# Performance work log

Hardware: AMD Instinct MI355X
Metric: run time of the kernel (lower is better)

The kernel has to match this reference:

```python
import jax, jax.numpy as jnp
import numpy as np

N_BUCKETS = 512
SLOTS_PER_BUCKET = 32
TAU = 0.1
ALPHA = 0.5


def _l2norm(x, eps=1e-12):
    return x / jnp.maximum(jnp.linalg.norm(x, axis=-1, keepdims=True), eps)


def setup_inputs() -> dict:
    key = jax.random.key(0)
    ks = jax.random.split(key, 6)
    B, T, D = 2, 2048, 1024
    total_slots = N_BUCKETS * SLOTS_PER_BUCKET
    vocab = 50257
    query_emb = jax.random.normal(ks[0], (B, T, D), dtype=jnp.float32)
    tids = jax.random.randint(ks[1], (B, T), 0, vocab)
    slot_keys = jax.random.normal(ks[2], (total_slots, D), dtype=jnp.float32)
    slot_values = jax.random.normal(ks[3], (total_slots, D), dtype=jnp.float32)
    slot_tids = jax.random.randint(ks[4], (total_slots,), 0, vocab)
    centroid_codebook = _l2norm(jax.random.normal(ks[5], (N_BUCKETS, D), dtype=jnp.float32))
    return {
        "query_emb": query_emb,
        "tids": tids,
        "slot_keys": slot_keys,
        "slot_values": slot_values,
        "slot_tids": slot_tids,
        "centroid_codebook": centroid_codebook,
    }


def reference(query_emb, tids, slot_keys, slot_values, slot_tids, centroid_codebook):
    # CentroidAddressableManifold.read
    buckets = tids % N_BUCKETS                                  # [B,T]
    lex_anchors = centroid_codebook[buckets]                    # [B,T,D]
    q_norm = _l2norm(query_emb)
    # bucket-indexed gather of 32 slots per token
    indices = buckets[..., None] * SLOTS_PER_BUCKET + jnp.arange(SLOTS_PER_BUCKET)  # [B,T,S]
    b_keys = slot_keys[indices]                                 # [B,T,S,D]
    b_vals = slot_values[indices]                               # [B,T,S,D]
    unified_query = _l2norm(ALPHA * q_norm + (1.0 - ALPHA) * lex_anchors)
    scores = jnp.einsum("btd,btsd->bts", unified_query, b_keys)  # [B,T,S]
    # hard-match path
    gathered_tids = slot_tids[indices]                          # [B,T,S]
    match_mask = (tids[..., None] == gathered_tids).astype(scores.dtype)
    match_sum = match_mask.sum(axis=-1, keepdims=True)
    has_match = match_sum > 0
    probs_hard = match_mask / (match_sum + 1e-9)
    probs_soft = jax.nn.softmax(scores / TAU, axis=-1)
    val_hard = jnp.einsum("bts,btsw->btw", probs_hard, b_vals)
    val_soft = jnp.einsum("bts,btsw->btw", probs_soft, b_vals)
    val_out = jnp.where(has_match, val_hard, val_soft)          # [B,T,D]
    return val_out
```

## Files before the change

kernel.cpp:

```cpp
#include <hip/hip_runtime.h>

#define NB 512
#define SLOTS 32
#define D 1024
#define D4 256
#define TC 8
#define CAP 64
#define TAU_INV 10.0f
#define BT 512

__global__ void k_zero(int* __restrict__ cnt) {
    if (threadIdx.x < NB) cnt[threadIdx.x] = 0;
}

__global__ void k_build(const int* __restrict__ tids, int n,
                        int* __restrict__ cnt, int* __restrict__ list) {
    int i = blockIdx.x * 256 + threadIdx.x;
    if (i < n) {
        int b = tids[i] & (NB - 1);
        int p = atomicAdd(&cnt[b], 1);
        if (p < CAP) list[b * CAP + p] = i;
    }
}

__global__ __launch_bounds__(BT, 2)
void k_main(const float* __restrict__ query,
            const int*   __restrict__ tids,
            const float* __restrict__ skeys,
            const float* __restrict__ svals,
            const int*   __restrict__ stids,
            const float* __restrict__ centroid,
            float*       __restrict__ out,
            const int*   __restrict__ cnt,
            const int*   __restrict__ list)
{
    const int bucket = blockIdx.x & (NB - 1);
    const int part   = blockIdx.x >> 9;
    const int tidx   = threadIdx.x;
    const int lane   = tidx & 63;
    const int wid    = tidx >> 6;

    const int count = min(cnt[bucket], CAP);
    const int ncnt  = (count - part + 1) >> 1;
    if (ncnt <= 0) return;

    __shared__ float s_uq[TC][D];
    __shared__ float s_scores[TC][SLOTS];
    __shared__ float s_probs[TC][SLOTS];
    __shared__ int   s_tok[TC];
    __shared__ int   s_ttid[TC];

    const int slot_tid = stids[bucket * SLOTS + (lane & 31)];
    const float4* kb = (const float4*)(skeys + (size_t)bucket * SLOTS * D);
    const float4* vb = (const float4*)(svals + (size_t)bucket * SLOTS * D);
    const float4* cb = (const float4*)(centroid + (size_t)bucket * D);

    for (int c0 = 0; c0 < ncnt; c0 += TC) {
        const int nt = min(TC, ncnt - c0);

        if (wid < nt) {
            const int tok = list[bucket * CAP + part + 2 * (c0 + wid)];
            const float4* q4 = (const float4*)(query + (size_t)tok * D);
            float4 qv[4], anc[4];
            float ss = 0.f;
            #pragma unroll
            for (int j = 0; j < 4; ++j) {
                qv[j]  = q4[lane + 64 * j];
                anc[j] = cb[lane + 64 * j];
                ss += qv[j].x*qv[j].x + qv[j].y*qv[j].y + qv[j].z*qv[j].z + qv[j].w*qv[j].w;
            }
            #pragma unroll
            for (int off = 32; off >= 1; off >>= 1) ss += __shfl_xor(ss, off);
            const float qn = 0.5f / fmaxf(sqrtf(ss), 1e-12f);
            float4 uv[4];
            float ss2 = 0.f;
            #pragma unroll
            for (int j = 0; j < 4; ++j) {
                uv[j].x = qv[j].x * qn + 0.5f * anc[j].x;
                uv[j].y = qv[j].y * qn + 0.5f * anc[j].y;
                uv[j].z = qv[j].z * qn + 0.5f * anc[j].z;
                uv[j].w = qv[j].w * qn + 0.5f * anc[j].w;
                ss2 += uv[j].x*uv[j].x + uv[j].y*uv[j].y + uv[j].z*uv[j].z + uv[j].w*uv[j].w;
            }
            #pragma unroll
            for (int off = 32; off >= 1; off >>= 1) ss2 += __shfl_xor(ss2, off);
            const float un = 1.0f / fmaxf(sqrtf(ss2), 1e-12f);
            #pragma unroll
            for (int j = 0; j < 4; ++j) {
                ((float4*)s_uq[wid])[lane + 64 * j] =
                    make_float4(uv[j].x*un, uv[j].y*un, uv[j].z*un, uv[j].w*un);
            }
            if (lane == 0) { s_tok[wid] = tok; s_ttid[wid] = tids[tok]; }
        }
        __syncthreads();

        {
            const int sbase = wid * 4;
            const float4* kr = kb + (size_t)sbase * D4;
            float4 k0[4], k1[4], k2[4], k3[4];
            #pragma unroll
            for (int j = 0; j < 4; ++j) {
                k0[j] = kr[0 * D4 + lane + 64 * j];
                k1[j] = kr[1 * D4 + lane + 64 * j];
                k2[j] = kr[2 * D4 + lane + 64 * j];
                k3[j] = kr[3 * D4 + lane + 64 * j];
            }
            for (int t = 0; t < nt; ++t) {
                const float4* u4 = (const float4*)s_uq[t];
                float P0 = 0.f, P1 = 0.f, P2 = 0.f, P3 = 0.f;
                #pragma unroll
                for (int j = 0; j < 4; ++j) {
                    float4 u = u4[lane + 64 * j];
                    P0 += k0[j].x*u.x + k0[j].y*u.y + k0[j].z*u.z + k0[j].w*u.w;
                    P1 += k1[j].x*u.x + k1[j].y*u.y + k1[j].z*u.z + k1[j].w*u.w;
                    P2 += k2[j].x*u.x + k2[j].y*u.y + k2[j].z*u.z + k2[j].w*u.w;
                    P3 += k3[j].x*u.x + k3[j].y*u.y + k3[j].z*u.z + k3[j].w*u.w;
                }
                {
                    const bool hi = (lane & 1) != 0;
                    const float sA = hi ? P0 : P2, kA = hi ? P2 : P0;
                    P0 = kA + __shfl_xor(sA, 1);
                    const float sB = hi ? P1 : P3, kB = hi ? P3 : P1;
                    P1 = kB + __shfl_xor(sB, 1);
                }
                {
                    const bool hi = (lane & 2) != 0;
                    const float sA = hi ? P0 : P1, kA = hi ? P1 : P0;
                    P0 = kA + __shfl_xor(sA, 2);
                }
                P0 += __shfl_xor(P0, 4);
                P0 += __shfl_xor(P0, 8);
                P0 += __shfl_xor(P0, 16);
                P0 += __shfl_xor(P0, 32);
                if (lane < 4)
                    s_scores[t][sbase + (((lane & 1) << 1) | ((lane >> 1) & 1))] = P0;
            }
        }
        __syncthreads();

        if (wid < nt && lane < 32) {
            const float sc = s_scores[wid][lane];
            float mx = sc;
            #pragma unroll
            for (int off = 16; off >= 1; off >>= 1) mx = fmaxf(mx, __shfl_xor(mx, off));
            const float e = __expf((sc - mx) * TAU_INV);
            const float f = (slot_tid == s_ttid[wid]) ? 1.f : 0.f;
            float es = e, ms = f;
            #pragma unroll
            for (int off = 16; off >= 1; off >>= 1) {
                es += __shfl_xor(es, off);
                ms += __shfl_xor(ms, off);
            }
            s_probs[wid][lane] = (ms > 0.f) ? f / (ms + 1e-9f) : e / es;
        }
        __syncthreads();

        {
            const int col = tidx & 255;
            const int grp = tidx >> 8;
            float4 acc[4];
            #pragma unroll
            for (int k = 0; k < 4; ++k) acc[k] = make_float4(0.f, 0.f, 0.f, 0.f);

            #pragma unroll 1
            for (int s0 = 0; s0 < SLOTS; s0 += 8) {
                float4 v[8];
                #pragma unroll
                for (int i = 0; i < 8; ++i) v[i] = vb[(s0 + i) * D4 + col];
                #pragma unroll
                for (int k = 0; k < 4; ++k) {
                    const int t = grp * 4 + k;
                    if (t < nt) {
                        const float4 pA = ((const float4*)s_probs[t])[(s0 >> 2) + 0];
                        const float4 pB = ((const float4*)s_probs[t])[(s0 >> 2) + 1];
                        acc[k].x += pA.x*v[0].x + pA.y*v[1].x + pA.z*v[2].x + pA.w*v[3].x
                                  + pB.x*v[4].x + pB.y*v[5].x + pB.z*v[6].x + pB.w*v[7].x;
                        acc[k].y += pA.x*v[0].y + pA.y*v[1].y + pA.z*v[2].y + pA.w*v[3].y
                                  + pB.x*v[4].y + pB.y*v[5].y + pB.z*v[6].y + pB.w*v[7].y;
                        acc[k].z += pA.x*v[0].z + pA.y*v[1].z + pA.z*v[2].z + pA.w*v[3].z
                                  + pB.x*v[4].z + pB.y*v[5].z + pB.z*v[6].z + pB.w*v[7].z;
                        acc[k].w += pA.x*v[0].w + pA.y*v[1].w + pA.z*v[2].w + pA.w*v[3].w
                                  + pB.x*v[4].w + pB.y*v[5].w + pB.z*v[6].w + pB.w*v[7].w;
                    }
                }
            }
            #pragma unroll
            for (int k = 0; k < 4; ++k) {
                const int t = grp * 4 + k;
                if (t < nt) {
                    ((float4*)(out + (size_t)s_tok[t] * D))[col] = acc[k];
                }
            }
        }
        if (c0 + TC < ncnt) __syncthreads();
    }
}

extern "C" void kernel_launch(void* const* d_in, const int* in_sizes, int n_in,
                              void* d_out, int out_size, void* d_ws, size_t ws_size,
                              hipStream_t stream) {
    const float* query    = (const float*)d_in[0];
    const int*   tids     = (const int*)  d_in[1];
    const float* skeys    = (const float*)d_in[2];
    const float* svals    = (const float*)d_in[3];
    const int*   stids    = (const int*)  d_in[4];
    const float* centroid = (const float*)d_in[5];
    float* out = (float*)d_out;
    const int n_tokens = in_sizes[1];

    int* cnt  = (int*)d_ws;
    int* list = cnt + NB;

    k_zero<<<1, 512, 0, stream>>>(cnt);
    k_build<<<(n_tokens + 255) / 256, 256, 0, stream>>>(tids, n_tokens, cnt, list);
    k_main<<<NB * 2, BT, 0, stream>>>(query, tids, skeys, svals, stids,
                                      centroid, out, cnt, list);
}
```

Baseline: 65.37 us.

## Precompute unified queries in separate kernel and drop shared-memory staging

Moves the query/centroid normalisation into a new per-token kernel, k_uq, that writes the unified query vectors into the output buffer. The main kernel then reads each token's unified query straight from global memory during scoring and overwrites the same rows with the final values. This removes the 32 KB shared-memory staging buffer and the per-chunk normalisation step, which should allow more blocks per CU. The costs are an extra launch, an extra round trip through global memory for the unified queries, repeated reads of them by every wave, and reliance on in-place aliasing of the output buffer.

Measured after the change: 71.25 us. +9.0%, slower.

```diff
diff --git a/kernel.cpp b/kernel.cpp
--- a/kernel.cpp
+++ b/kernel.cpp
@@ -23,14 +23,59 @@
     }
 }
 
+__global__ __launch_bounds__(256, 2)
+void k_uq(const float* __restrict__ query,
+          const int*   __restrict__ tids,
+          const float* __restrict__ centroid,
+          float*       __restrict__ uq_out,
+          int n_tokens)
+{
+    const int lane = threadIdx.x & 63;
+    const int wid  = threadIdx.x >> 6;
+    const int tok  = blockIdx.x * 4 + wid;
+    if (tok >= n_tokens) return;
+
+    const int b = tids[tok] & (NB - 1);
+    const float4* q4 = (const float4*)(query + (size_t)tok * D);
+    const float4* cb = (const float4*)(centroid + (size_t)b * D);
+
+    float4 qv[4], anc[4];
+    float ss = 0.f;
+    #pragma unroll
+    for (int j = 0; j < 4; ++j) {
+        qv[j]  = q4[lane + 64 * j];
+        anc[j] = cb[lane + 64 * j];
+        ss += qv[j].x*qv[j].x + qv[j].y*qv[j].y + qv[j].z*qv[j].z + qv[j].w*qv[j].w;
+    }
+    #pragma unroll
+    for (int off = 32; off >= 1; off >>= 1) ss += __shfl_xor(ss, off);
+    const float qn = 0.5f / fmaxf(sqrtf(ss), 1e-12f);
+    float4 uv[4];
+    float ss2 = 0.f;
+    #pragma unroll
+    for (int j = 0; j < 4; ++j) {
+        uv[j].x = qv[j].x * qn + 0.5f * anc[j].x;
+        uv[j].y = qv[j].y * qn + 0.5f * anc[j].y;
+        uv[j].z = qv[j].z * qn + 0.5f * anc[j].z;
+        uv[j].w = qv[j].w * qn + 0.5f * anc[j].w;
+        ss2 += uv[j].x*uv[j].x + uv[j].y*uv[j].y + uv[j].z*uv[j].z + uv[j].w*uv[j].w;
+    }
+    #pragma unroll
+    for (int off = 32; off >= 1; off >>= 1) ss2 += __shfl_xor(ss2, off);
+    const float un = 1.0f / fmaxf(sqrtf(ss2), 1e-12f);
+    float4* o4 = (float4*)(uq_out + (size_t)tok * D);
+    #pragma unroll
+    for (int j = 0; j < 4; ++j)
+        o4[lane + 64 * j] = make_float4(uv[j].x*un, uv[j].y*un, uv[j].z*un, uv[j].w*un);
+}
+
 __global__ __launch_bounds__(BT, 2)
-void k_main(const float* __restrict__ query,
-            const int*   __restrict__ tids,
+void k_main(const int*   __restrict__ tids,
+            const float*              uq,
             const float* __restrict__ skeys,
             const float* __restrict__ svals,
             const int*   __restrict__ stids,
-            const float* __restrict__ centroid,
-            float*       __restrict__ out,
+            float*                    out,
             const int*   __restrict__ cnt,
             const int*   __restrict__ list)
 {
@@ -44,7 +89,6 @@
     const int ncnt  = (count - part + 1) >> 1;
     if (ncnt <= 0) return;
 
-    __shared__ float s_uq[TC][D];
     __shared__ float s_scores[TC][SLOTS];
     __shared__ float s_probs[TC][SLOTS];
     __shared__ int   s_tok[TC];
@@ -53,44 +97,14 @@
     const int slot_tid = stids[bucket * SLOTS + (lane & 31)];
     const float4* kb = (const float4*)(skeys + (size_t)bucket * SLOTS * D);
     const float4* vb = (const float4*)(svals + (size_t)bucket * SLOTS * D);
-    const float4* cb = (const float4*)(centroid + (size_t)bucket * D);
 
     for (int c0 = 0; c0 < ncnt; c0 += TC) {
         const int nt = min(TC, ncnt - c0);
 
-        if (wid < nt) {
-            const int tok = list[bucket * CAP + part + 2 * (c0 + wid)];
-            const float4* q4 = (const float4*)(query + (size_t)tok * D);
-            float4 qv[4], anc[4];
-            float ss = 0.f;
-            #pragma unroll
-            for (int j = 0; j < 4; ++j) {
-                qv[j]  = q4[lane + 64 * j];
-                anc[j] = cb[lane + 64 * j];
-                ss += qv[j].x*qv[j].x + qv[j].y*qv[j].y + qv[j].z*qv[j].z + qv[j].w*qv[j].w;
-            }
-            #pragma unroll
-            for (int off = 32; off >= 1; off >>= 1) ss += __shfl_xor(ss, off);
-            const float qn = 0.5f / fmaxf(sqrtf(ss), 1e-12f);
-            float4 uv[4];
-            float ss2 = 0.f;
-            #pragma unroll
-            for (int j = 0; j < 4; ++j) {
-                uv[j].x = qv[j].x * qn + 0.5f * anc[j].x;
-                uv[j].y = qv[j].y * qn + 0.5f * anc[j].y;
-                uv[j].z = qv[j].z * qn + 0.5f * anc[j].z;
-                uv[j].w = qv[j].w * qn + 0.5f * anc[j].w;
-                ss2 += uv[j].x*uv[j].x + uv[j].y*uv[j].y + uv[j].z*uv[j].z + uv[j].w*uv[j].w;
-            }
-            #pragma unroll
-            for (int off = 32; off >= 1; off >>= 1) ss2 += __shfl_xor(ss2, off);
-            const float un = 1.0f / fmaxf(sqrtf(ss2), 1e-12f);
-            #pragma unroll
-            for (int j = 0; j < 4; ++j) {
-                ((float4*)s_uq[wid])[lane + 64 * j] =
-                    make_float4(uv[j].x*un, uv[j].y*un, uv[j].z*un, uv[j].w*un);
-            }
-            if (lane == 0) { s_tok[wid] = tok; s_ttid[wid] = tids[tok]; }
+        if (tidx < nt) {
+            const int tok = list[bucket * CAP + part + 2 * (c0 + tidx)];
+            s_tok[tidx]  = tok;
+            s_ttid[tidx] = tids[tok];
         }
         __syncthreads();
 
@@ -106,7 +120,7 @@
                 k3[j] = kr[3 * D4 + lane + 64 * j];
             }
             for (int t = 0; t < nt; ++t) {
-                const float4* u4 = (const float4*)s_uq[t];
+                const float4* u4 = (const float4*)(uq + (size_t)s_tok[t] * D);
                 float P0 = 0.f, P1 = 0.f, P2 = 0.f, P3 = 0.f;
                 #pragma unroll
                 for (int j = 0; j < 4; ++j) {
@@ -213,6 +227,7 @@
 
     k_zero<<<1, 512, 0, stream>>>(cnt);
     k_build<<<(n_tokens + 255) / 256, 256, 0, stream>>>(tids, n_tokens, cnt, list);
-    k_main<<<NB * 2, BT, 0, stream>>>(query, tids, skeys, svals, stids,
-                                      centroid, out, cnt, list);
-}
+    k_uq<<<(n_tokens + 3) / 4, 256, 0, stream>>>(query, tids, centroid, out, n_tokens);
+    k_main<<<NB * 2, BT, 0, stream>>>(tids, out, skeys, svals, stids,
+                                      out, cnt, list);
+}
```
